# Performance work log

Hardware: AMD Instinct MI355X
Metric: run time of the kernel (lower is better)

The kernel has to match this reference:

```python
import jax, jax.numpy as jnp
import numpy as np

N_NODES = 100000
N_EDGES = 3200000
D_IN = 128
D_OUT = 128
EPS = 0.0  # GINConv default eps, not trained


def setup_inputs() -> dict:
    key = jax.random.key(0)
    k1, k2, k3, k4, k5, k6, k7 = jax.random.split(key, 7)
    x = jax.random.normal(k1, (N_NODES, D_IN), dtype=jnp.float32)
    edge_index = jax.random.randint(k2, (2, N_EDGES), 0, N_NODES, dtype=jnp.int64)
    # MLP params: Linear(D_IN->D_OUT), ReLU, Linear(D_OUT->D_OUT)
    s1 = 1.0 / np.sqrt(D_IN)
    s2 = 1.0 / np.sqrt(D_OUT)
    W1 = jax.random.uniform(k3, (D_IN, D_OUT), jnp.float32, -s1, s1)
    b1 = jax.random.uniform(k4, (D_OUT,), jnp.float32, -s1, s1)
    W2 = jax.random.uniform(k5, (D_OUT, D_OUT), jnp.float32, -s2, s2)
    b2 = jax.random.uniform(k6, (D_OUT,), jnp.float32, -s2, s2)
    return {"x": x, "edge_index": edge_index, "W1": W1, "b1": b1, "W2": W2, "b2": b2}


def reference(x, edge_index, W1, b1, W2, b2):
    src, dst = edge_index[0], edge_index[1]
    # message = x[src]; aggregate by sum onto dst (source_to_target flow)
    agg = jax.ops.segment_sum(x[src], dst, num_segments=x.shape[0])  # [N, D_IN]
    h = (1.0 + EPS) * x + agg
    h = jax.nn.relu(h @ W1 + b1)
    return h @ W2 + b2
```

## Files before the change

kernel.cpp:

```cpp
#include <hip/hip_runtime.h>

#define D 128
#define TILE_ROWS 64
#define MLP_THREADS 512
#define BK_NODES 128
#define MAX_BKT 1024
#define EPB 16
#define PRO_THREADS 256
#define CAST_VEC 4
#define SC_THREADS 512
#define SC_EPB 24
#define BC_THREADS 512
#define CAPL 6144
#define FMLP_THREADS 512
#define MLP_BM 128
#define HSTR 136

typedef unsigned short ushort_t;
typedef unsigned int uint_t;
typedef __attribute__((ext_vector_type(8))) short short8v;
typedef __attribute__((ext_vector_type(4))) float f32x4;

__device__ __forceinline__ ushort_t f2bf(float f) {
    uint_t u = __float_as_uint(f);
    u = u + 0x7FFFu + ((u >> 16) & 1u);
    return (ushort_t)(u >> 16);
}
__device__ __forceinline__ float bf_lo(uint_t u) { return __uint_as_float(u << 16); }
__device__ __forceinline__ float bf_hi(uint_t u) { return __uint_as_float(u & 0xffff0000u); }

__global__ __launch_bounds__(PRO_THREADS) void prologue_kernel(
    const float* __restrict__ x, ushort_t* __restrict__ xh, int n4, int cast_blocks,
    const int* __restrict__ dsts, int* __restrict__ ghist, int ne, int nbkt, int hist_blocks,
    const float* __restrict__ W1, const float* __restrict__ W2,
    ushort_t* __restrict__ w1t, ushort_t* __restrict__ w2t) {
    __shared__ int h[MAX_BKT];
    int b = blockIdx.x;
    if (b < cast_blocks) {
        int base = b * PRO_THREADS * CAST_VEC + threadIdx.x;
#pragma unroll
        for (int j = 0; j < CAST_VEC; ++j) {
            int i = base + j * PRO_THREADS;
            if (i < n4) {
                float4 v = reinterpret_cast<const float4*>(x)[i];
                ushort4 o;
                o.x = f2bf(v.x); o.y = f2bf(v.y); o.z = f2bf(v.z); o.w = f2bf(v.w);
                reinterpret_cast<ushort4*>(xh)[i] = o;
            }
        }
        return;
    }
    b -= cast_blocks;
    if (b < hist_blocks) {
        for (int k = threadIdx.x; k < nbkt; k += PRO_THREADS) h[k] = 0;
        __syncthreads();
        int base = b * PRO_THREADS * EPB;
        for (int j = 0; j < EPB; ++j) {
            int e = base + j * PRO_THREADS + threadIdx.x;
            if (e < ne) atomicAdd(&h[dsts[e] >> 7], 1);
        }
        __syncthreads();
        for (int k = threadIdx.x; k < nbkt; k += PRO_THREADS)
            if (h[k]) atomicAdd(&ghist[k], h[k]);
        return;
    }
    b -= hist_blocks;
    int i = b * PRO_THREADS + threadIdx.x;
    if (w1t != nullptr && i < D * D) {
        int c = i & 127, k = i >> 7;
        w1t[(size_t)c * HSTR + k] = f2bf(W1[(size_t)k * D + c]);
        w2t[(size_t)c * HSTR + k] = f2bf(W2[(size_t)k * D + c]);
    }
}

__global__ __launch_bounds__(SC_THREADS) void coarse_scatter_kernel(
    const int* __restrict__ ei, const int* __restrict__ ghist,
    int* __restrict__ cbase, int* __restrict__ ccursor,
    int* __restrict__ offsets, int* __restrict__ pairs,
    int ne, int nbkt, int nnodes) {
    __shared__ int h[MAX_BKT];
    __shared__ int cbl[MAX_BKT];
    __shared__ int lbase[MAX_BKT];
    __shared__ int gbase[MAX_BKT];
    __shared__ int lcur[MAX_BKT];
    __shared__ int stot[SC_THREADS];
    __shared__ int stage[SC_THREADS * SC_EPB];

    const int t = threadIdx.x;
    const int base = blockIdx.x * SC_THREADS * SC_EPB;

    int g0 = (2 * t < nbkt) ? ghist[2 * t] : 0;
    int g1 = (2 * t + 1 < nbkt) ? ghist[2 * t + 1] : 0;
    stot[t] = g0 + g1;
    __syncthreads();
    for (int off = 1; off < SC_THREADS; off <<= 1) {
        int u = (t >= off) ? stot[t - off] : 0;
        __syncthreads();
        stot[t] += u;
        __syncthreads();
    }
    {
        int ge = stot[t] - (g0 + g1);
        cbl[2 * t] = ge;
        cbl[2 * t + 1] = ge + g0;
        if (blockIdx.x == 0) {
            if (2 * t < nbkt) cbase[2 * t] = ge;
            if (2 * t + 1 < nbkt) cbase[2 * t + 1] = ge + g0;
            if (t == SC_THREADS - 1) { cbase[nbkt] = stot[t]; offsets[nnodes] = ne; }
        }
    }
    __syncthreads();

    for (int k = t; k < MAX_BKT; k += SC_THREADS) h[k] = 0;
    __syncthreads();
    for (int j = 0; j < SC_EPB; ++j) {
        int e = base + j * SC_THREADS + t;
        if (e < ne) atomicAdd(&h[ei[ne + e] >> 7], 1);
    }
    __syncthreads();

    int a0 = h[2 * t], a1 = h[2 * t + 1];
    stot[t] = a0 + a1;
    __syncthreads();
    for (int off = 1; off < SC_THREADS; off <<= 1) {
        int u = (t >= off) ? stot[t - off] : 0;
        __syncthreads();
        stot[t] += u;
        __syncthreads();
    }
    int bexc = stot[t] - (a0 + a1);
    lbase[2 * t] = bexc;          lcur[2 * t] = bexc;
    lbase[2 * t + 1] = bexc + a0; lcur[2 * t + 1] = bexc + a0;
    __syncthreads();

    for (int k = t; k < MAX_BKT; k += SC_THREADS)
        gbase[k] = h[k] ? (cbl[k] + atomicAdd(&ccursor[k], h[k])) : 0;
    __syncthreads();

    for (int j = 0; j < SC_EPB; ++j) {
        int e = base + j * SC_THREADS + t;
        if (e < ne) {
            int dst = ei[ne + e];
            int src = ei[e];
            int k = dst >> 7;
            int pos = atomicAdd(&lcur[k], 1);
            stage[pos] = (src << 7) | (dst & (BK_NODES - 1));
        }
    }
    __syncthreads();

    const int lane = t & 63, w = t >> 6;
    for (int k = w; k < nbkt; k += (SC_THREADS / 64)) {
        int cnt = h[k];
        int lb = lbase[k], gb = gbase[k];
        for (int i = lane; i < cnt; i += 64)
            pairs[gb + i] = stage[lb + i];
    }
}

__global__ __launch_bounds__(BC_THREADS) void bucket_csr_kernel(
    const int* __restrict__ pairs, const int* __restrict__ cbase,
    int* __restrict__ offsets, int* __restrict__ sorted_src, int nnodes) {
    __shared__ int h[BK_NODES];
    __shared__ int ex[BK_NODES];
    __shared__ int cur[BK_NODES];
    __shared__ int stage[CAPL];
    int b = blockIdx.x;
    int t = threadIdx.x;
    int rbeg = cbase[b], rend = cbase[b + 1];
    int cnt = rend - rbeg;
    if (t < BK_NODES) h[t] = 0;
    __syncthreads();
    for (int i = rbeg + t; i < rend; i += blockDim.x)
        atomicAdd(&h[pairs[i] & (BK_NODES - 1)], 1);
    __syncthreads();
    if (t < BK_NODES) ex[t] = h[t];
    __syncthreads();
    for (int off = 1; off < BK_NODES; off <<= 1) {
        int u = (t >= off && t < BK_NODES) ? ex[t - off] : 0;
        __syncthreads();
        if (t < BK_NODES) ex[t] += u;
        __syncthreads();
    }
    const bool staged = (cnt <= CAPL);
    if (t < BK_NODES) {
        int e = ex[t] - h[t];
        cur[t] = staged ? e : rbeg + e;
        int node = b * BK_NODES + t;
        if (node < nnodes) offsets[node] = rbeg + e;
    }
    __syncthreads();
    if (staged) {
        for (int i = rbeg + t; i < rend; i += blockDim.x) {
            int p = pairs[i];
            int pos = atomicAdd(&cur[p & (BK_NODES - 1)], 1);
            stage[pos] = p >> 7;
        }
        __syncthreads();
        for (int i = t; i < cnt; i += blockDim.x)
            sorted_src[rbeg + i] = stage[i];
    } else {
        for (int i = rbeg + t; i < rend; i += blockDim.x) {
            int p = pairs[i];
            int pos = atomicAdd(&cur[p & (BK_NODES - 1)], 1);
            sorted_src[pos] = p >> 7;
        }
    }
}

__global__ void agg_bf_kernel(const ushort_t* __restrict__ xh,
                              const int* __restrict__ sorted_src,
                              const int* __restrict__ offsets,
                              float* __restrict__ out,
                              uint_t* __restrict__ hbf, int nnodes) {
    int gid = blockIdx.x * blockDim.x + threadIdx.x;
    int node = gid >> 6;
    if (node >= nnodes) return;
    const int lane = threadIdx.x & 63;
    const int col = lane & 31;
    const int half = lane >> 5;
    const uint2* xp = reinterpret_cast<const uint2*>(xh);
    int beg = offsets[node];
    int end = offsets[node + 1];

    float s0, s1, s2, s3;
    {
        uint2 u = xp[(size_t)node * 32 + col];
        if (half) { u.x = 0u; u.y = 0u; }
        s0 = bf_lo(u.x); s1 = bf_hi(u.x);
        s2 = bf_lo(u.y); s3 = bf_hi(u.y);
    }

    int i = beg;
    for (; i + 16 <= end; i += 16) {
        uint2 v0 = xp[(size_t)sorted_src[i + 0 + half] * 32 + col];
        uint2 v1 = xp[(size_t)sorted_src[i + 2 + half] * 32 + col];
        uint2 v2 = xp[(size_t)sorted_src[i + 4 + half] * 32 + col];
        uint2 v3 = xp[(size_t)sorted_src[i + 6 + half] * 32 + col];
        uint2 v4 = xp[(size_t)sorted_src[i + 8 + half] * 32 + col];
        uint2 v5 = xp[(size_t)sorted_src[i + 10 + half] * 32 + col];
        uint2 v6 = xp[(size_t)sorted_src[i + 12 + half] * 32 + col];
        uint2 v7 = xp[(size_t)sorted_src[i + 14 + half] * 32 + col];
        s0 += bf_lo(v0.x) + bf_lo(v1.x) + bf_lo(v2.x) + bf_lo(v3.x) +
              bf_lo(v4.x) + bf_lo(v5.x) + bf_lo(v6.x) + bf_lo(v7.x);
        s1 += bf_hi(v0.x) + bf_hi(v1.x) + bf_hi(v2.x) + bf_hi(v3.x) +
              bf_hi(v4.x) + bf_hi(v5.x) + bf_hi(v6.x) + bf_hi(v7.x);
        s2 += bf_lo(v0.y) + bf_lo(v1.y) + bf_lo(v2.y) + bf_lo(v3.y) +
              bf_lo(v4.y) + bf_lo(v5.y) + bf_lo(v6.y) + bf_lo(v7.y);
        s3 += bf_hi(v0.y) + bf_hi(v1.y) + bf_hi(v2.y) + bf_hi(v3.y) +
              bf_hi(v4.y) + bf_hi(v5.y) + bf_hi(v6.y) + bf_hi(v7.y);
    }
    for (; i + 2 <= end; i += 2) {
        uint2 u = xp[(size_t)sorted_src[i + half] * 32 + col];
        s0 += bf_lo(u.x); s1 += bf_hi(u.x);
        s2 += bf_lo(u.y); s3 += bf_hi(u.y);
    }
    if (i < end && half == 0) {
        uint2 u = xp[(size_t)sorted_src[i] * 32 + col];
        s0 += bf_lo(u.x); s1 += bf_hi(u.x);
        s2 += bf_lo(u.y); s3 += bf_hi(u.y);
    }

    s0 += __shfl_xor(s0, 32);
    s1 += __shfl_xor(s1, 32);
    s2 += __shfl_xor(s2, 32);
    s3 += __shfl_xor(s3, 32);

    if (half == 0) {
        if (hbf) {
            uint_t lo = (uint_t)f2bf(s0) | ((uint_t)f2bf(s1) << 16);
            uint_t hi = (uint_t)f2bf(s2) | ((uint_t)f2bf(s3) << 16);
            uint2 o; o.x = lo; o.y = hi;
            reinterpret_cast<uint2*>(hbf)[(size_t)node * 32 + col] = o;
        } else {
            float4 o; o.x = s0; o.y = s1; o.z = s2; o.w = s3;
            reinterpret_cast<float4*>(out + (size_t)node * D)[col] = o;
        }
    }
}

__global__ void agg_fp_kernel(const float* __restrict__ x,
                              const int* __restrict__ sorted_src,
                              const int* __restrict__ offsets,
                              float* __restrict__ out, int nnodes) {
    int gid = blockIdx.x * blockDim.x + threadIdx.x;
    int node = gid >> 6;
    if (node >= nnodes) return;
    int lane = threadIdx.x & 63;
    int beg = offsets[node];
    int end = offsets[node + 1];
    const float2* xp = reinterpret_cast<const float2*>(x);
    float2 a = xp[(size_t)node * 64 + lane];
    float sx = a.x, sy = a.y;
    int i = beg;
    for (; i + 8 <= end; i += 8) {
        int s0 = sorted_src[i + 0], s1 = sorted_src[i + 1];
        int s2 = sorted_src[i + 2], s3 = sorted_src[i + 3];
        int s4 = sorted_src[i + 4], s5 = sorted_src[i + 5];
        int s6 = sorted_src[i + 6], s7 = sorted_src[i + 7];
        float2 v0 = xp[(size_t)s0 * 64 + lane];
        float2 v1 = xp[(size_t)s1 * 64 + lane];
        float2 v2 = xp[(size_t)s2 * 64 + lane];
        float2 v3 = xp[(size_t)s3 * 64 + lane];
        float2 v4 = xp[(size_t)s4 * 64 + lane];
        float2 v5 = xp[(size_t)s5 * 64 + lane];
        float2 v6 = xp[(size_t)s6 * 64 + lane];
        float2 v7 = xp[(size_t)s7 * 64 + lane];
        sx += ((v0.x + v1.x) + (v2.x + v3.x)) + ((v4.x + v5.x) + (v6.x + v7.x));
        sy += ((v0.y + v1.y) + (v2.y + v3.y)) + ((v4.y + v5.y) + (v6.y + v7.y));
    }
    for (; i < end; ++i) {
        float2 v = xp[(size_t)sorted_src[i] * 64 + lane];
        sx += v.x;
        sy += v.y;
    }
    float2 o; o.x = sx; o.y = sy;
    reinterpret_cast<float2*>(out)[(size_t)node * 64 + lane] = o;
}

template <bool BF>
__global__ __launch_bounds__(FMLP_THREADS, 1) void fused_mlp_kernel(
    const float* __restrict__ h, const uint_t* __restrict__ hbf,
    const ushort_t* __restrict__ w1t, const ushort_t* __restrict__ w2t,
    const float* __restrict__ b1, const float* __restrict__ b2,
    float* __restrict__ outp, int nrows) {
    __shared__ ushort_t sh[MLP_BM * HSTR];
    __shared__ ushort_t sw1[D * HSTR];
    __shared__ ushort_t sw2[D * HSTR];
    const int tid = threadIdx.x;
    const int row0 = blockIdx.x * MLP_BM;

    {
        const uint4* s1 = reinterpret_cast<const uint4*>(w1t);
        const uint4* s2 = reinterpret_cast<const uint4*>(w2t);
        uint4* d1 = reinterpret_cast<uint4*>(sw1);
        uint4* d2 = reinterpret_cast<uint4*>(sw2);
        for (int i = tid; i < D * HSTR / 8; i += FMLP_THREADS) { d1[i] = s1[i]; d2[i] = s2[i]; }
    }
    if (BF) {
        for (int i = tid; i < MLP_BM * 16; i += FMLP_THREADS) {
            int r = i >> 4, c = i & 15;
            uint4 v = make_uint4(0u, 0u, 0u, 0u);
            if (row0 + r < nrows)
                v = reinterpret_cast<const uint4*>(hbf + (size_t)(row0 + r) * 64)[c];
            *reinterpret_cast<uint4*>(&sh[r * HSTR + c * 8]) = v;
        }
    } else {
        for (int i = tid; i < MLP_BM * 32; i += FMLP_THREADS) {
            int r = i >> 5, c4 = i & 31;
            float4 v = make_float4(0.f, 0.f, 0.f, 0.f);
            if (row0 + r < nrows)
                v = reinterpret_cast<const float4*>(h + (size_t)(row0 + r) * D)[c4];
            ushort4 o;
            o.x = f2bf(v.x); o.y = f2bf(v.y); o.z = f2bf(v.z); o.w = f2bf(v.w);
            *reinterpret_cast<ushort4*>(&sh[r * HSTR + c4 * 4]) = o;
        }
    }
    __syncthreads();

    const int w = tid >> 6, l = tid & 63;
    const int lr = l & 15, lg = l >> 4;
    const int rowb = w * 16;

    short8v A[4];
#pragma unroll
    for (int kk = 0; kk < 4; ++kk)
        A[kk] = *reinterpret_cast<const short8v*>(&sh[(rowb + lr) * HSTR + kk * 32 + lg * 8]);
#pragma unroll
    for (int n = 0; n < 8; ++n) {
        float bv = b1[n * 16 + lr];
        f32x4 acc = {bv, bv, bv, bv};
#pragma unroll
        for (int kk = 0; kk < 4; ++kk) {
            short8v B = *reinterpret_cast<const short8v*>(&sw1[(n * 16 + lr) * HSTR + kk * 32 + lg * 8]);
            acc = __builtin_amdgcn_mfma_f32_16x16x32_bf16(A[kk], B, acc, 0, 0, 0);
        }
#pragma unroll
        for (int r = 0; r < 4; ++r) {
            float v = fmaxf(acc[r], 0.f);
            sh[(rowb + lg * 4 + r) * HSTR + n * 16 + lr] = f2bf(v);
        }
    }

    short8v A2[4];
#pragma unroll
    for (int kk = 0; kk < 4; ++kk)
        A2[kk] = *reinterpret_cast<const short8v*>(&sh[(rowb + lr) * HSTR + kk * 32 + lg * 8]);
#pragma unroll
    for (int n = 0; n < 8; ++n) {
        float bv = b2[n * 16 + lr];
        f32x4 acc = {bv, bv, bv, bv};
#pragma unroll
        for (int kk = 0; kk < 4; ++kk) {
            short8v B = *reinterpret_cast<const short8v*>(&sw2[(n * 16 + lr) * HSTR + kk * 32 + lg * 8]);
            acc = __builtin_amdgcn_mfma_f32_16x16x32_bf16(A2[kk], B, acc, 0, 0, 0);
        }
#pragma unroll
        for (int r = 0; r < 4; ++r) {
            int grow = row0 + rowb + lg * 4 + r;
            if (grow < nrows)
                outp[(size_t)grow * D + n * 16 + lr] = acc[r];
        }
    }
}

__global__ void init_kernel(const float* __restrict__ x, float* __restrict__ out, int n4) {
    int i = blockIdx.x * blockDim.x + threadIdx.x;
    if (i < n4) {
        reinterpret_cast<float4*>(out)[i] = reinterpret_cast<const float4*>(x)[i];
    }
}

__global__ void scatter_kernel(const float* __restrict__ x,
                               const int* __restrict__ ei,
                               float* __restrict__ out, int ne) {
    long long gid = (long long)blockIdx.x * blockDim.x + threadIdx.x;
    int e = (int)(gid >> 5);
    if (e >= ne) return;
    int d0 = ((int)gid & 31) * 4;
    int src = ei[e];
    int dst = ei[ne + e];
    float4 v = *reinterpret_cast<const float4*>(x + (long long)src * D + d0);
    float* o = out + (long long)dst * D + d0;
    atomicAdd(o + 0, v.x);
    atomicAdd(o + 1, v.y);
    atomicAdd(o + 2, v.z);
    atomicAdd(o + 3, v.w);
}

template <bool RELU>
__global__ __launch_bounds__(MLP_THREADS, 1) void mlp_kernel(
    const float* __restrict__ in, const float* __restrict__ W,
    const float* __restrict__ b, float* __restrict__ outp, int nrows) {
    __shared__ float Wl[D][D];
    __shared__ float inl[TILE_ROWS][D + 4];

    const int tid = threadIdx.x;
    const int row0 = blockIdx.x * TILE_ROWS;

    for (int i = tid; i < D * D / 4; i += MLP_THREADS) {
        reinterpret_cast<float4*>(&Wl[0][0])[i] =
            reinterpret_cast<const float4*>(W)[i];
    }
    for (int i = tid; i < TILE_ROWS * (D / 4); i += MLP_THREADS) {
        int r = i >> 5;
        int k4 = i & 31;
        float4 v = make_float4(0.f, 0.f, 0.f, 0.f);
        if (row0 + r < nrows)
            v = *reinterpret_cast<const float4*>(in + (size_t)(row0 + r) * D + 4 * k4);
        *reinterpret_cast<float4*>(&inl[r][4 * k4]) = v;
    }
    __syncthreads();

    const int cg = tid & 31;
    const int rg = tid >> 5;
    const int c0 = cg * 4;
    const int r0 = rg * 4;

    float4 bv = *reinterpret_cast<const float4*>(b + c0);
    float acc[4][4];
#pragma unroll
    for (int i = 0; i < 4; ++i) {
        acc[i][0] = bv.x; acc[i][1] = bv.y; acc[i][2] = bv.z; acc[i][3] = bv.w;
    }

#pragma unroll 4
    for (int k4 = 0; k4 < 32; ++k4) {
        float4 w0 = *reinterpret_cast<const float4*>(&Wl[4 * k4 + 0][c0]);
        float4 w1 = *reinterpret_cast<const float4*>(&Wl[4 * k4 + 1][c0]);
        float4 w2 = *reinterpret_cast<const float4*>(&Wl[4 * k4 + 2][c0]);
        float4 w3 = *reinterpret_cast<const float4*>(&Wl[4 * k4 + 3][c0]);
#pragma unroll
        for (int i = 0; i < 4; ++i) {
            float4 a = *reinterpret_cast<const float4*>(&inl[r0 + i][4 * k4]);
            acc[i][0] += a.x * w0.x + a.y * w1.x + a.z * w2.x + a.w * w3.x;
            acc[i][1] += a.x * w0.y + a.y * w1.y + a.z * w2.y + a.w * w3.y;
            acc[i][2] += a.x * w0.z + a.y * w1.z + a.z * w2.z + a.w * w3.z;
            acc[i][3] += a.x * w0.w + a.y * w1.w + a.z * w2.w + a.w * w3.w;
        }
    }

#pragma unroll
    for (int i = 0; i < 4; ++i) {
        int r = row0 + r0 + i;
        if (r < nrows) {
            float4 o;
            if (RELU) {
                o.x = fmaxf(acc[i][0], 0.f); o.y = fmaxf(acc[i][1], 0.f);
                o.z = fmaxf(acc[i][2], 0.f); o.w = fmaxf(acc[i][3], 0.f);
            } else {
                o.x = acc[i][0]; o.y = acc[i][1]; o.z = acc[i][2]; o.w = acc[i][3];
            }
            *reinterpret_cast<float4*>(outp + (size_t)r * D + c0) = o;
        }
    }
}

extern "C" void kernel_launch(void* const* d_in, const int* in_sizes, int n_in,
                              void* d_out, int out_size, void* d_ws, size_t ws_size,
                              hipStream_t stream) {
    const float* x = (const float*)d_in[0];
    const int* ei = (const int*)d_in[1];
    const float* W1 = (const float*)d_in[2];
    const float* b1 = (const float*)d_in[3];
    const float* W2 = (const float*)d_in[4];
    const float* b2 = (const float*)d_in[5];
    float* out = (float*)d_out;

    const int nrows = in_sizes[0] / D;
    const int ne = in_sizes[1] / 2;
    const int nbkt = (nrows + BK_NODES - 1) / BK_NODES;

    size_t xh_bytes = (((size_t)nrows * D * sizeof(ushort_t)) + 15) & ~(size_t)15;
    size_t csr_bytes = ((size_t)(nrows + 1) + 2 * (size_t)ne + 3 * (size_t)nbkt + 1) * sizeof(int);
    size_t need_fp = csr_bytes;
    size_t need_bf = xh_bytes + csr_bytes;
    size_t wt_bytes = (size_t)D * HSTR * sizeof(ushort_t);
    size_t wt_off = (need_bf + 15) & ~(size_t)15;
    size_t need_mfma = wt_off + 2 * wt_bytes;
    size_t hbf_off = (need_mfma + 15) & ~(size_t)15;
    size_t hbf_bytes = (size_t)nrows * D * sizeof(ushort_t);
    size_t need_hbf = hbf_off + hbf_bytes;

    const int n4 = nrows * (D / 4);
    const int hist_blocks = (ne + PRO_THREADS * EPB - 1) / (PRO_THREADS * EPB);
    const int sc_blocks = (ne + SC_THREADS * SC_EPB - 1) / (SC_THREADS * SC_EPB);

    bool use_mfma = false;
    bool use_hbf = false;
    ushort_t* w1t = nullptr;
    ushort_t* w2t = nullptr;
    uint_t* hbf = nullptr;

    if (nbkt <= MAX_BKT && ws_size >= need_fp) {
        const bool bf = (ws_size >= need_bf);
        use_mfma = (ws_size >= need_mfma);
        use_hbf = bf && use_mfma && (ws_size >= need_hbf);
        char* wp = (char*)d_ws;
        ushort_t* xh = nullptr;
        if (bf) { xh = (ushort_t*)wp; wp += xh_bytes; }
        int* offsets = (int*)wp;
        int* sorted_src = offsets + (nrows + 1);
        int* pairs = sorted_src + ne;
        int* ghist = pairs + ne;
        int* cbase = ghist + nbkt;
        int* ccursor = cbase + (nbkt + 1);
        if (use_mfma) {
            w1t = (ushort_t*)((char*)d_ws + wt_off);
            w2t = (ushort_t*)((char*)d_ws + wt_off + wt_bytes);
        }
        if (use_hbf) hbf = (uint_t*)((char*)d_ws + hbf_off);

        hipMemsetAsync(ghist, 0, (size_t)(3 * nbkt + 1) * sizeof(int), stream);

        const int cast_blocks = bf ? (n4 + PRO_THREADS * CAST_VEC - 1) / (PRO_THREADS * CAST_VEC) : 0;
        const int wprep_blocks = use_mfma ? (D * D + PRO_THREADS - 1) / PRO_THREADS : 0;
        const int pro_blocks = cast_blocks + hist_blocks + wprep_blocks;
        prologue_kernel<<<pro_blocks, PRO_THREADS, 0, stream>>>(
            x, xh, n4, cast_blocks, ei + ne, ghist, ne, nbkt, hist_blocks,
            W1, W2, w1t, w2t);

        coarse_scatter_kernel<<<sc_blocks, SC_THREADS, 0, stream>>>(
            ei, ghist, cbase, ccursor, offsets, pairs, ne, nbkt, nrows);
        bucket_csr_kernel<<<nbkt, BC_THREADS, 0, stream>>>(pairs, cbase, offsets, sorted_src, nrows);

        long long athreads = (long long)nrows * 64;
        int ablocks = (int)((athreads + 255) / 256);
        if (bf)
            agg_bf_kernel<<<ablocks, 256, 0, stream>>>(xh, sorted_src, offsets, out, hbf, nrows);
        else
            agg_fp_kernel<<<ablocks, 256, 0, stream>>>(x, sorted_src, offsets, out, nrows);
    } else {
        init_kernel<<<(n4 + 255) / 256, 256, 0, stream>>>(x, out, n4);
        long long sthreads = (long long)ne * 32;
        scatter_kernel<<<(int)((sthreads + 255) / 256), 256, 0, stream>>>(x, ei, out, ne);
    }

    if (use_mfma) {
        int fblocks = (nrows + MLP_BM - 1) / MLP_BM;
        if (use_hbf)
            fused_mlp_kernel<true><<<fblocks, FMLP_THREADS, 0, stream>>>(
                out, hbf, w1t, w2t, b1, b2, out, nrows);
        else
            fused_mlp_kernel<false><<<fblocks, FMLP_THREADS, 0, stream>>>(
                out, nullptr, w1t, w2t, b1, b2, out, nrows);
    } else {
        int mblocks = (nrows + TILE_ROWS - 1) / TILE_ROWS;
        mlp_kernel<true><<<mblocks, MLP_THREADS, 0, stream>>>(out, W1, b1, out, nrows);
        mlp_kernel<false><<<mblocks, MLP_THREADS, 0, stream>>>(out, W2, b2, out, nrows);
    }
}
```

Measured before the change: 241.4 us.

## Use wave-shuffle scans and single-pass edge loads in the bucket scatter kernels

Result: no change. 241.9 us (+0.2%).

```diff
diff --git a/kernel.cpp b/kernel.cpp
--- a/kernel.cpp
+++ b/kernel.cpp
@@ -9,7 +9,7 @@
 #define PRO_THREADS 256
 #define CAST_VEC 4
 #define SC_THREADS 512
-#define SC_EPB 24
+#define SC_EPB 12
 #define BC_THREADS 512
 #define CAPL 6144
 #define FMLP_THREADS 512
@@ -83,78 +83,92 @@
     __shared__ int lbase[MAX_BKT];
     __shared__ int gbase[MAX_BKT];
     __shared__ int lcur[MAX_BKT];
-    __shared__ int stot[SC_THREADS];
+    __shared__ int wtot[SC_THREADS / 64];
+    __shared__ int btot_s;
     __shared__ int stage[SC_THREADS * SC_EPB];
+    __shared__ ushort_t stagek[SC_THREADS * SC_EPB];
 
     const int t = threadIdx.x;
-    const int base = blockIdx.x * SC_THREADS * SC_EPB;
+    const int lane = t & 63, w = t >> 6;
+    const int base = blockIdx.x * (SC_THREADS * SC_EPB);
 
     int g0 = (2 * t < nbkt) ? ghist[2 * t] : 0;
     int g1 = (2 * t + 1 < nbkt) ? ghist[2 * t + 1] : 0;
-    stot[t] = g0 + g1;
-    __syncthreads();
-    for (int off = 1; off < SC_THREADS; off <<= 1) {
-        int u = (t >= off) ? stot[t - off] : 0;
-        __syncthreads();
-        stot[t] += u;
-        __syncthreads();
-    }
+    int sA = g0 + g1;
+#pragma unroll
+    for (int off = 1; off < 64; off <<= 1) {
+        int u = __shfl_up(sA, off);
+        if (lane >= off) sA += u;
+    }
+    if (lane == 63) wtot[w] = sA;
+    h[2 * t] = 0;
+    h[2 * t + 1] = 0;
+    __syncthreads();
     {
-        int ge = stot[t] - (g0 + g1);
-        cbl[2 * t] = ge;
-        cbl[2 * t + 1] = ge + g0;
+        int wb = 0;
+        for (int i = 0; i < w; ++i) wb += wtot[i];
+        int ex = wb + sA - (g0 + g1);
+        cbl[2 * t] = ex;
+        cbl[2 * t + 1] = ex + g0;
         if (blockIdx.x == 0) {
-            if (2 * t < nbkt) cbase[2 * t] = ge;
-            if (2 * t + 1 < nbkt) cbase[2 * t + 1] = ge + g0;
-            if (t == SC_THREADS - 1) { cbase[nbkt] = stot[t]; offsets[nnodes] = ne; }
-        }
-    }
-    __syncthreads();
-
-    for (int k = t; k < MAX_BKT; k += SC_THREADS) h[k] = 0;
-    __syncthreads();
+            if (2 * t < nbkt) cbase[2 * t] = ex;
+            if (2 * t + 1 < nbkt) cbase[2 * t + 1] = ex + g0;
+            if (t == SC_THREADS - 1) { cbase[nbkt] = wb + sA; offsets[nnodes] = ne; }
+        }
+    }
+
+    int karr[SC_EPB];
+    int parr[SC_EPB];
+#pragma unroll
     for (int j = 0; j < SC_EPB; ++j) {
         int e = base + j * SC_THREADS + t;
-        if (e < ne) atomicAdd(&h[ei[ne + e] >> 7], 1);
-    }
-    __syncthreads();
-
-    int a0 = h[2 * t], a1 = h[2 * t + 1];
-    stot[t] = a0 + a1;
-    __syncthreads();
-    for (int off = 1; off < SC_THREADS; off <<= 1) {
-        int u = (t >= off) ? stot[t - off] : 0;
-        __syncthreads();
-        stot[t] += u;
-        __syncthreads();
-    }
-    int bexc = stot[t] - (a0 + a1);
-    lbase[2 * t] = bexc;          lcur[2 * t] = bexc;
-    lbase[2 * t + 1] = bexc + a0; lcur[2 * t + 1] = bexc + a0;
-    __syncthreads();
-
-    for (int k = t; k < MAX_BKT; k += SC_THREADS)
-        gbase[k] = h[k] ? (cbl[k] + atomicAdd(&ccursor[k], h[k])) : 0;
-    __syncthreads();
-
-    for (int j = 0; j < SC_EPB; ++j) {
-        int e = base + j * SC_THREADS + t;
+        karr[j] = -1;
+        parr[j] = 0;
         if (e < ne) {
             int dst = ei[ne + e];
             int src = ei[e];
-            int k = dst >> 7;
-            int pos = atomicAdd(&lcur[k], 1);
-            stage[pos] = (src << 7) | (dst & (BK_NODES - 1));
-        }
-    }
-    __syncthreads();
-
-    const int lane = t & 63, w = t >> 6;
-    for (int k = w; k < nbkt; k += (SC_THREADS / 64)) {
-        int cnt = h[k];
-        int lb = lbase[k], gb = gbase[k];
-        for (int i = lane; i < cnt; i += 64)
-            pairs[gb + i] = stage[lb + i];
+            karr[j] = dst >> 7;
+            parr[j] = (src << 7) | (dst & (BK_NODES - 1));
+            atomicAdd(&h[karr[j]], 1);
+        }
+    }
+    __syncthreads();
+
+    int a0 = h[2 * t], a1 = h[2 * t + 1];
+    int sC = a0 + a1;
+#pragma unroll
+    for (int off = 1; off < 64; off <<= 1) {
+        int u = __shfl_up(sC, off);
+        if (lane >= off) sC += u;
+    }
+    if (lane == 63) wtot[w] = sC;
+    __syncthreads();
+    {
+        int wb = 0;
+        for (int i = 0; i < w; ++i) wb += wtot[i];
+        int ex = wb + sC - (a0 + a1);
+        lbase[2 * t] = ex;          lcur[2 * t] = ex;
+        lbase[2 * t + 1] = ex + a0; lcur[2 * t + 1] = ex + a0;
+        if (t == SC_THREADS - 1) btot_s = wb + sC;
+        gbase[2 * t] = a0 ? (cbl[2 * t] + atomicAdd(&ccursor[2 * t], a0)) : 0;
+        gbase[2 * t + 1] = a1 ? (cbl[2 * t + 1] + atomicAdd(&ccursor[2 * t + 1], a1)) : 0;
+    }
+    __syncthreads();
+
+#pragma unroll
+    for (int j = 0; j < SC_EPB; ++j) {
+        if (karr[j] >= 0) {
+            int pos = atomicAdd(&lcur[karr[j]], 1);
+            stage[pos] = parr[j];
+            stagek[pos] = (ushort_t)karr[j];
+        }
+    }
+    __syncthreads();
+
+    const int btot = btot_s;
+    for (int i = t; i < btot; i += SC_THREADS) {
+        int k = stagek[i];
+        pairs[gbase[k] + (i - lbase[k])] = stage[i];
     }
 }
 
@@ -174,17 +188,22 @@
     for (int i = rbeg + t; i < rend; i += blockDim.x)
         atomicAdd(&h[pairs[i] & (BK_NODES - 1)], 1);
     __syncthreads();
-    if (t < BK_NODES) ex[t] = h[t];
-    __syncthreads();
-    for (int off = 1; off < BK_NODES; off <<= 1) {
-        int u = (t >= off && t < BK_NODES) ? ex[t - off] : 0;
-        __syncthreads();
-        if (t < BK_NODES) ex[t] += u;
-        __syncthreads();
-    }
+    if (t < 64) {
+        int b0 = h[2 * t], b1 = h[2 * t + 1];
+        int s = b0 + b1;
+#pragma unroll
+        for (int off = 1; off < 64; off <<= 1) {
+            int u = __shfl_up(s, off);
+            if (t >= off) s += u;
+        }
+        int e0 = s - (b0 + b1);
+        ex[2 * t] = e0;
+        ex[2 * t + 1] = e0 + b0;
+    }
+    __syncthreads();
     const bool staged = (cnt <= CAPL);
     if (t < BK_NODES) {
-        int e = ex[t] - h[t];
+        int e = ex[t];
         cur[t] = staged ? e : rbeg + e;
         int node = b * BK_NODES + t;
         if (node < nnodes) offsets[node] = rbeg + e;
```
